# Kernel optimization log

Hardware: AMD Instinct MI355X
Metric: run time of the kernel (lower is better)

## Reference

```python
import jax, jax.numpy as jnp
import numpy as np

B, S, D = 8, 2048, 256
H, DFF, L = 8, 1024, 5
DK = D // H
EPS = 1e-5


def _xavier(key, shape):
    fan_in, fan_out = shape[-2], shape[-1]
    a = jnp.sqrt(6.0 / (fan_in + fan_out))
    return jax.random.uniform(key, shape, jnp.float32, -a, a)


def setup_inputs() -> dict:
    key = jax.random.key(0)
    ks = jax.random.split(key, 12)
    inp = {
        "src": jax.random.normal(ks[0], (B, S, D), jnp.float32),
        "sph": jax.random.normal(ks[1], (B, S, S), jnp.float32),
        # stacked per-layer parameters, leading dim = L
        "Wq": _xavier(ks[2], (L, D, D)), "bq": jnp.zeros((L, D), jnp.float32),
        "Wk": _xavier(ks[3], (L, D, D)), "bk": jnp.zeros((L, D), jnp.float32),
        "Wv": _xavier(ks[4], (L, D, D)), "bv": jnp.zeros((L, D), jnp.float32),
        "Wo": _xavier(ks[5], (L, D, D)), "bo": jnp.zeros((L, D), jnp.float32),
        "W1": _xavier(ks[6], (L, D, DFF)), "b1": jnp.zeros((L, DFF), jnp.float32),
        "W2": _xavier(ks[7], (L, DFF, D)), "b2": jnp.zeros((L, D), jnp.float32),
        "ln1_g": jnp.ones((L, D), jnp.float32), "ln1_b": jnp.zeros((L, D), jnp.float32),
        "ln2_g": jnp.ones((L, D), jnp.float32), "ln2_b": jnp.zeros((L, D), jnp.float32),
    }
    return inp


def _layernorm(x, g, b):
    mu = jnp.mean(x, axis=-1, keepdims=True)
    var = jnp.mean(jnp.square(x - mu), axis=-1, keepdims=True)
    return (x - mu) * jax.lax.rsqrt(var + EPS) * g + b


def _layer(x, sph, Wq, bq, Wk, bk, Wv, bv, Wo, bo, W1, b1, W2, b2, g1, be1, g2, be2):
    # multihead attention with additive sph score bias
    q = (x @ Wq + bq).reshape(B, S, H, DK)
    k = (x @ Wk + bk).reshape(B, S, H, DK)
    v = (x @ Wv + bv).reshape(B, S, H, DK)
    scores = jnp.einsum("bqhd,bkhd->bhqk", q, k) / jnp.sqrt(jnp.float32(DK))
    scores = scores + sph[:, None, :, :]  # bias broadcast over heads
    attn = jax.nn.softmax(scores, axis=-1)
    ctx = jnp.einsum("bhqk,bkhd->bqhd", attn, v).reshape(B, S, D)
    src2 = ctx @ Wo + bo
    x = _layernorm(x + src2, g1, be1)
    # FFN (exact gelu, matching torch F.gelu default)
    h = jax.nn.gelu(x @ W1 + b1, approximate=False)
    src2 = h @ W2 + b2
    x = _layernorm(x + src2, g2, be2)
    return x


def reference(src, sph, Wq, bq, Wk, bk, Wv, bv, Wo, bo, W1, b1, W2, b2, ln1_g, ln1_b, ln2_g, ln2_b):
    x = src
    for i in range(L):
        x = _layer(x, sph, Wq[i], bq[i], Wk[i], bk[i], Wv[i], bv[i], Wo[i], bo[i],
                   W1[i], b1[i], W2[i], b2[i], ln1_g[i], ln1_b[i], ln2_g[i], ln2_b[i])
    return x
```

## Files before the change

### kernel.cpp

```cpp
#include <hip/hip_runtime.h>
#include <cstdint>

__device__ __forceinline__ float b2f(unsigned short u) {
    unsigned int t = ((unsigned int)u) << 16;
    float f;
    __builtin_memcpy(&f, &t, 4);
    return f;
}
__device__ __forceinline__ unsigned short f2b(float f) {
    unsigned int u;
    __builtin_memcpy(&u, &f, 4);
    unsigned int r = (u + 0x7FFFu + ((u >> 16) & 1u)) >> 16;
    return (unsigned short)r;
}
__device__ __forceinline__ float2 bpair(unsigned int u) {
    float2 r;
    unsigned int lo = u << 16;
    unsigned int hi = u & 0xFFFF0000u;
    __builtin_memcpy(&r.x, &lo, 4);
    __builtin_memcpy(&r.y, &hi, 4);
    return r;
}

typedef __attribute__((ext_vector_type(8))) short bf16x8;
typedef __attribute__((ext_vector_type(4))) float f32x4;

#define LOG2E 1.4426950408889634f
#define SC2   0.2550348595f

__device__ __forceinline__ void gload16(const void* g, void* l) {
    __builtin_amdgcn_global_load_lds(
        (const __attribute__((address_space(1))) unsigned int*)g,
        (__attribute__((address_space(3))) unsigned int*)l, 16, 0, 0);
}

__global__ void transcvt_k(const float* __restrict__ in,
                           unsigned short* __restrict__ out, int R, int C,
                           int in_z, int out_z) {
    __shared__ float tile[32][33];
    in += (size_t)blockIdx.z * in_z;
    out += (size_t)blockIdx.z * out_z;
    const int c0 = blockIdx.x * 32, r0 = blockIdx.y * 32;
    const int tx = threadIdx.x, ty = threadIdx.y;
#pragma unroll
    for (int i = 0; i < 32; i += 8)
        tile[ty + i][tx] = in[(size_t)(r0 + ty + i) * C + c0 + tx];
    __syncthreads();
#pragma unroll
    for (int i = 0; i < 32; i += 8)
        out[(size_t)(c0 + ty + i) * R + r0 + tx] = f2b(tile[tx][ty + i]);
}

__global__ __launch_bounds__(256) void sph_cvt(const float* __restrict__ in,
                                               unsigned short* __restrict__ out) {
    const size_t idx = (size_t)blockIdx.x * 256 + threadIdx.x;
    const float4 a = ((const float4*)in)[idx * 2];
    const float4 b = ((const float4*)in)[idx * 2 + 1];
    uint4 o;
    o.x = (unsigned)f2b(a.x * LOG2E) | ((unsigned)f2b(a.y * LOG2E) << 16);
    o.y = (unsigned)f2b(a.z * LOG2E) | ((unsigned)f2b(a.w * LOG2E) << 16);
    o.z = (unsigned)f2b(b.x * LOG2E) | ((unsigned)f2b(b.y * LOG2E) << 16);
    o.w = (unsigned)f2b(b.z * LOG2E) | ((unsigned)f2b(b.w * LOG2E) << 16);
    ((uint4*)out)[idx] = o;
}

__global__ __launch_bounds__(256) void cvt_bf16_k(const float* __restrict__ in,
                                                  unsigned short* __restrict__ out) {
    const size_t idx = (size_t)blockIdx.x * 256 + threadIdx.x;
    const float4 a = ((const float4*)in)[idx * 2];
    const float4 b = ((const float4*)in)[idx * 2 + 1];
    uint4 o;
    o.x = (unsigned)f2b(a.x) | ((unsigned)f2b(a.y) << 16);
    o.y = (unsigned)f2b(a.z) | ((unsigned)f2b(a.w) << 16);
    o.z = (unsigned)f2b(b.x) | ((unsigned)f2b(b.y) << 16);
    o.w = (unsigned)f2b(b.z) | ((unsigned)f2b(b.w) << 16);
    ((uint4*)out)[idx] = o;
}

template <int TN, int QKVB>
__global__ __launch_bounds__(256) void gemm_gl_kernel(
    const unsigned short* __restrict__ A, const unsigned short* __restrict__ Wt,
    const float* __restrict__ biasQ, const float* __restrict__ biasK,
    const float* __restrict__ biasV, unsigned short* __restrict__ C,
    int M, int N, int K, int do_gelu) {
    constexpr int JN = TN / 32;
    constexpr int NCH = 16 + TN / 8;
    __shared__ unsigned short As[128 * 64];
    __shared__ unsigned short Bs[TN * 64];
    const int tid = threadIdx.x;
    const int lane = tid & 63, wid = tid >> 6;
    const int m0 = blockIdx.y * 128, n0 = blockIdx.x * TN;
    const int wm = (wid >> 1) * 64, wn = (wid & 1) * (TN / 2);
    const int quad = lane >> 4, mrow = lane & 15;
    const int lrow = lane >> 3, lslot = lane & 7;
    f32x4 acc[4][JN] = {};

    for (int kb = 0; kb < K; kb += 64) {
#pragma unroll
        for (int cc = 0; cc < NCH / 4; ++cc) {
            const int c = wid * (NCH / 4) + cc;
            if (c < 16) {
                const int row = c * 8 + lrow;
                const int gcol = ((lslot ^ (row & 7)) << 3) + kb;
                gload16(A + (size_t)(m0 + row) * K + gcol, &As[c * 512 + lane * 8]);
            } else {
                const int row = (c - 16) * 8 + lrow;
                const int gcol = ((lslot ^ (row & 7)) << 3) + kb;
                gload16(Wt + (size_t)(n0 + row) * K + gcol, &Bs[(c - 16) * 512 + lane * 8]);
            }
        }
        __syncthreads();
#pragma unroll
        for (int h = 0; h < 2; ++h) {
            bf16x8 af[4], bfr[JN];
#pragma unroll
            for (int i = 0; i < 4; i++) {
                const int ar = wm + i * 16 + mrow;
                af[i] = *(const bf16x8*)&As[ar * 64 + (((h * 4 + quad) ^ (ar & 7)) << 3)];
            }
#pragma unroll
            for (int j = 0; j < JN; j++) {
                const int br = wn + j * 16 + mrow;
                bfr[j] = *(const bf16x8*)&Bs[br * 64 + (((h * 4 + quad) ^ (br & 7)) << 3)];
            }
#pragma unroll
            for (int i = 0; i < 4; i++)
#pragma unroll
                for (int j = 0; j < JN; j++)
                    acc[i][j] = __builtin_amdgcn_mfma_f32_16x16x32_bf16(af[i], bfr[j], acc[i][j], 0, 0, 0);
        }
        __syncthreads();
    }

    const float* bp;
    if (QKVB) {
        const int bsel = n0 >> 8;
        bp = bsel == 0 ? biasQ : (bsel == 1 ? biasK : biasV);
    } else {
        bp = biasQ;
    }
#pragma unroll
    for (int i = 0; i < 4; i++)
#pragma unroll
        for (int j = 0; j < JN; j++) {
            const int col = n0 + wn + j * 16 + mrow;
            const float bv = QKVB ? bp[col & 255] : bp[col];
#pragma unroll
            for (int r = 0; r < 4; r++) {
                const int row = m0 + wm + i * 16 + quad * 4 + r;
                float v = acc[i][j][r] + bv;
                if (do_gelu) v = 0.5f * v * (1.0f + erff(v * 0.70710678118654752f));
                C[(size_t)row * N + col] = f2b(v);
            }
        }
}

template <int SPHB16>
__global__ __launch_bounds__(256) void attn_mfma(
    const unsigned short* __restrict__ Qb, const unsigned short* __restrict__ Kb,
    const unsigned short* __restrict__ Vb, const float* __restrict__ sphf,
    const unsigned short* __restrict__ sphb, unsigned short* __restrict__ Ctx) {
    __shared__ unsigned short Ks[64 * 40];
    __shared__ unsigned short Vt[32 * 72];
    __shared__ unsigned short Ps[4][16 * 72];

    const int tid = threadIdx.x, lane = tid & 63, wid = tid >> 6;
    const int quad = lane >> 4, lq = lane & 15;
    const int bid = blockIdx.x;
    const int h = bid >> 8, b = (bid >> 5) & 7, qt = bid & 31;
    const int q0 = qt * 64;
    const size_t bS = (size_t)b * 2048;

    const int skey = tid >> 2, sdg = (tid & 3) << 3;
    const unsigned short* kgp = Kb + (bS + skey) * 768 + h * 32 + sdg;
    const int vkp = tid & 31, vdg = (tid >> 5) << 2;
    const unsigned short* vgp = Vb + (bS + 2 * vkp) * 768 + h * 32 + vdg;

    const bf16x8 qf = *(const bf16x8*)(Qb + (bS + q0 + wid * 16 + lq) * 768 + h * 32 + quad * 8);

    const size_t sprow = ((size_t)b * 2048 + q0 + wid * 16 + quad * 4) * 2048 + lq;
    const float* spf = sphf + sprow;
    const unsigned short* spb = sphb + sprow;

    float l_r[4] = {0.f, 0.f, 0.f, 0.f};
    f32x4 o0 = {}, o1 = {};

    for (int kt = 0; kt < 32; ++kt) {
        const int k0 = kt * 64;
        __syncthreads();
        *(uint4*)&Ks[skey * 40 + sdg] = *(const uint4*)(kgp + (size_t)k0 * 768);
        {
            uint2 va = *(const uint2*)(vgp + (size_t)k0 * 768);
            uint2 vb2 = *(const uint2*)(vgp + (size_t)k0 * 768 + 768);
            *(unsigned int*)&Vt[(vdg + 0) * 72 + 2 * vkp] = (va.x & 0xFFFFu) | (vb2.x << 16);
            *(unsigned int*)&Vt[(vdg + 1) * 72 + 2 * vkp] = (va.x >> 16) | (vb2.x & 0xFFFF0000u);
            *(unsigned int*)&Vt[(vdg + 2) * 72 + 2 * vkp] = (va.y & 0xFFFFu) | (vb2.y << 16);
            *(unsigned int*)&Vt[(vdg + 3) * 72 + 2 * vkp] = (va.y >> 16) | (vb2.y & 0xFFFF0000u);
        }
        __syncthreads();

        const f32x4 zf = {};
        f32x4 sa0 = __builtin_amdgcn_mfma_f32_16x16x32_bf16(
            qf, *(const bf16x8*)&Ks[(0  + lq) * 40 + quad * 8], zf, 0, 0, 0);
        f32x4 sa1 = __builtin_amdgcn_mfma_f32_16x16x32_bf16(
            qf, *(const bf16x8*)&Ks[(16 + lq) * 40 + quad * 8], zf, 0, 0, 0);
        f32x4 sa2 = __builtin_amdgcn_mfma_f32_16x16x32_bf16(
            qf, *(const bf16x8*)&Ks[(32 + lq) * 40 + quad * 8], zf, 0, 0, 0);
        f32x4 sa3 = __builtin_amdgcn_mfma_f32_16x16x32_bf16(
            qf, *(const bf16x8*)&Ks[(48 + lq) * 40 + quad * 8], zf, 0, 0, 0);

#pragma unroll
        for (int r = 0; r < 4; ++r) {
            float sb0, sb1, sb2, sb3;
            if (SPHB16) {
                const unsigned short* spr = spb + (size_t)r * 2048 + k0;
                sb0 = b2f(spr[0]);  sb1 = b2f(spr[16]);
                sb2 = b2f(spr[32]); sb3 = b2f(spr[48]);
            } else {
                const float* spr = spf + (size_t)r * 2048 + k0;
                sb0 = spr[0]  * LOG2E; sb1 = spr[16] * LOG2E;
                sb2 = spr[32] * LOG2E; sb3 = spr[48] * LOG2E;
            }
            const float p0 = __builtin_amdgcn_exp2f(fmaf(sa0[r], SC2, sb0));
            const float p1 = __builtin_amdgcn_exp2f(fmaf(sa1[r], SC2, sb1));
            const float p2 = __builtin_amdgcn_exp2f(fmaf(sa2[r], SC2, sb2));
            const float p3 = __builtin_amdgcn_exp2f(fmaf(sa3[r], SC2, sb3));
            l_r[r] += (p0 + p1) + (p2 + p3);
            unsigned short* pw = &Ps[wid][(quad * 4 + r) * 72 + lq];
            pw[0]  = f2b(p0);
            pw[16] = f2b(p1);
            pw[32] = f2b(p2);
            pw[48] = f2b(p3);
        }

#pragma unroll
        for (int k2 = 0; k2 < 2; ++k2) {
            bf16x8 pf = *(const bf16x8*)&Ps[wid][lq * 72 + k2 * 32 + quad * 8];
            o0 = __builtin_amdgcn_mfma_f32_16x16x32_bf16(
                pf, *(const bf16x8*)&Vt[(0  + lq) * 72 + k2 * 32 + quad * 8], o0, 0, 0, 0);
            o1 = __builtin_amdgcn_mfma_f32_16x16x32_bf16(
                pf, *(const bf16x8*)&Vt[(16 + lq) * 72 + k2 * 32 + quad * 8], o1, 0, 0, 0);
        }
    }

    unsigned short* op = Ctx + (bS + q0 + wid * 16 + quad * 4) * 256 + h * 32;
#pragma unroll
    for (int r = 0; r < 4; ++r) {
        float l = l_r[r];
        l += __shfl_xor(l, 1);
        l += __shfl_xor(l, 2);
        l += __shfl_xor(l, 4);
        l += __shfl_xor(l, 8);
        const float inv = 1.f / l;
        op[r * 256 + lq]      = f2b(o0[r] * inv);
        op[r * 256 + 16 + lq] = f2b(o1[r] * inv);
    }
}

__global__ __launch_bounds__(256) void add_ln_kernel(
    const float* x, const unsigned short* r,
    const float* __restrict__ g, const float* __restrict__ be,
    float* out, unsigned short* xb) {
    const int lane = threadIdx.x & 63, wid = threadIdx.x >> 6;
    const size_t row = (size_t)blockIdx.x * 4 + wid;
    float4 xv = *(const float4*)(x + row * 256 + lane * 4);
    uint2 ru = *(const uint2*)(r + row * 256 + lane * 4);
    float2 ra = bpair(ru.x), rb = bpair(ru.y);
    float v[4] = {xv.x + ra.x, xv.y + ra.y, xv.z + rb.x, xv.w + rb.y};
    float sum = v[0] + v[1] + v[2] + v[3];
#pragma unroll
    for (int off = 32; off; off >>= 1) sum += __shfl_xor(sum, off);
    const float mu = sum * (1.f / 256.f);
    float sq = 0.f;
#pragma unroll
    for (int i = 0; i < 4; i++) { float d = v[i] - mu; sq += d * d; }
#pragma unroll
    for (int off = 32; off; off >>= 1) sq += __shfl_xor(sq, off);
    const float rs = rsqrtf(sq * (1.f / 256.f) + 1e-5f);
    float4 o;
    o.x = (v[0] - mu) * rs * g[lane * 4 + 0] + be[lane * 4 + 0];
    o.y = (v[1] - mu) * rs * g[lane * 4 + 1] + be[lane * 4 + 1];
    o.z = (v[2] - mu) * rs * g[lane * 4 + 2] + be[lane * 4 + 2];
    o.w = (v[3] - mu) * rs * g[lane * 4 + 3] + be[lane * 4 + 3];
    *(float4*)(out + row * 256 + lane * 4) = o;
    uint2 p;
    p.x = (unsigned)f2b(o.x) | ((unsigned)f2b(o.y) << 16);
    p.y = (unsigned)f2b(o.z) | ((unsigned)f2b(o.w) << 16);
    *(uint2*)(xb + row * 256 + lane * 4) = p;
}

extern "C" void kernel_launch(void* const* d_in, const int* in_sizes, int n_in,
                              void* d_out, int out_size, void* d_ws, size_t ws_size,
                              hipStream_t stream) {
    const float* src = (const float*)d_in[0];
    const float* sph = (const float*)d_in[1];
    const float* Wq  = (const float*)d_in[2];
    const float* bq  = (const float*)d_in[3];
    const float* Wk  = (const float*)d_in[4];
    const float* bk  = (const float*)d_in[5];
    const float* Wv  = (const float*)d_in[6];
    const float* bv  = (const float*)d_in[7];
    const float* Wo  = (const float*)d_in[8];
    const float* bo  = (const float*)d_in[9];
    const float* W1  = (const float*)d_in[10];
    const float* b1  = (const float*)d_in[11];
    const float* W2  = (const float*)d_in[12];
    const float* b2  = (const float*)d_in[13];
    const float* g1  = (const float*)d_in[14];
    const float* be1 = (const float*)d_in[15];
    const float* g2  = (const float*)d_in[16];
    const float* be2 = (const float*)d_in[17];

    char* ws = (char*)d_ws;
    float* X = (float*)d_out;
    unsigned short* QKV = (unsigned short*)(ws + 0);
    unsigned short* CTX = (unsigned short*)(ws + 25165824);
    unsigned short* T2  = (unsigned short*)(ws + 33554432);
    unsigned short* H   = QKV;
    unsigned short* XB  = T2;
    unsigned short* WtQKV = (unsigned short*)(ws + 41943040);
    unsigned short* WtO   = (unsigned short*)(ws + 43909120);
    unsigned short* Wt1   = (unsigned short*)(ws + 44564480);
    unsigned short* Wt2   = (unsigned short*)(ws + 47185920);
    unsigned short* SPHB  = (unsigned short*)(ws + 50331648);
    const int use_b16 = (ws_size >= (size_t)117440512);

    const dim3 tb(32, 8);
    transcvt_k<<<dim3(8, 8, 5),  tb, 0, stream>>>(Wq, WtQKV,          256, 256, 65536, 196608);
    transcvt_k<<<dim3(8, 8, 5),  tb, 0, stream>>>(Wk, WtQKV + 65536,  256, 256, 65536, 196608);
    transcvt_k<<<dim3(8, 8, 5),  tb, 0, stream>>>(Wv, WtQKV + 131072, 256, 256, 65536, 196608);
    transcvt_k<<<dim3(8, 8, 5),  tb, 0, stream>>>(Wo, WtO,            256, 256, 65536, 65536);
    transcvt_k<<<dim3(32, 8, 5), tb, 0, stream>>>(W1, Wt1,            256, 1024, 262144, 262144);
    transcvt_k<<<dim3(8, 32, 5), tb, 0, stream>>>(W2, Wt2,            1024, 256, 262144, 262144);
    if (use_b16) sph_cvt<<<16384, 256, 0, stream>>>(sph, SPHB);
    cvt_bf16_k<<<2048, 256, 0, stream>>>(src, XB);

    hipMemcpyAsync(X, src, 16777216, hipMemcpyDeviceToDevice, stream);

    const int M = 16384;
    for (int lyr = 0; lyr < 5; ++lyr) {
        gemm_gl_kernel<128, 1><<<dim3(6, 128), 256, 0, stream>>>(
            XB, WtQKV + lyr * 196608, bq + lyr * 256, bk + lyr * 256, bv + lyr * 256,
            QKV, M, 768, 256, 0);
        if (use_b16)
            attn_mfma<1><<<2048, 256, 0, stream>>>(QKV, QKV + 256, QKV + 512, sph, SPHB, CTX);
        else
            attn_mfma<0><<<2048, 256, 0, stream>>>(QKV, QKV + 256, QKV + 512, sph, SPHB, CTX);
        gemm_gl_kernel<64, 0><<<dim3(4, 128), 256, 0, stream>>>(
            CTX, WtO + lyr * 65536, bo + lyr * 256, nullptr, nullptr, T2, M, 256, 256, 0);
        add_ln_kernel<<<4096, 256, 0, stream>>>(X, T2, g1 + lyr * 256, be1 + lyr * 256, X, XB);
        gemm_gl_kernel<128, 0><<<dim3(8, 128), 256, 0, stream>>>(
            XB, Wt1 + lyr * 262144, b1 + lyr * 1024, nullptr, nullptr, H, M, 1024, 256, 1);
        gemm_gl_kernel<64, 0><<<dim3(4, 128), 256, 0, stream>>>(
            H, Wt2 + lyr * 262144, b2 + lyr * 256, nullptr, nullptr, T2, M, 256, 1024, 0);
        add_ln_kernel<<<4096, 256, 0, stream>>>(X, T2, g2 + lyr * 256, be2 + lyr * 256, X, XB);
    }
}
```

Measured before the change: 1.493 ms.

## Remap attention blocks, add MFMA priority hints, packed bf16 converts, fuse src copy

Attention blocks are remapped so consecutive block IDs fall on different (b,h) groups. The V-tile load is reordered so each pair of rows sits 16 apart, and K/V pointers are advanced incrementally. s_setprio is raised around the MFMA sections to favour matrix issue. Scalar bf16 rounding is replaced with packed hardware conversion in several kernels, and P is written as 32-bit pairs. The device-to-device memcpy of src is folded into the bf16 conversion kernel. The block remap changes L2 locality for sph and K/V, which could help or hurt.

```diff
diff --git a/kernel.cpp b/kernel.cpp
--- a/kernel.cpp
+++ b/kernel.cpp
@@ -1,4 +1,5 @@
 #include <hip/hip_runtime.h>
+#include <hip/hip_bf16.h>
 #include <cstdint>
 
 __device__ __forceinline__ float b2f(unsigned short u) {
@@ -12,6 +13,12 @@
     __builtin_memcpy(&u, &f, 4);
     unsigned int r = (u + 0x7FFFu + ((u >> 16) & 1u)) >> 16;
     return (unsigned short)r;
+}
+__device__ __forceinline__ unsigned int pkbf(float a, float b) {
+    __hip_bfloat162 t = __float22bfloat162_rn(float2{a, b});
+    unsigned int u;
+    __builtin_memcpy(&u, &t, 4);
+    return u;
 }
 __device__ __forceinline__ float2 bpair(unsigned int u) {
     float2 r;
@@ -57,24 +64,27 @@
     const float4 a = ((const float4*)in)[idx * 2];
     const float4 b = ((const float4*)in)[idx * 2 + 1];
     uint4 o;
-    o.x = (unsigned)f2b(a.x * LOG2E) | ((unsigned)f2b(a.y * LOG2E) << 16);
-    o.y = (unsigned)f2b(a.z * LOG2E) | ((unsigned)f2b(a.w * LOG2E) << 16);
-    o.z = (unsigned)f2b(b.x * LOG2E) | ((unsigned)f2b(b.y * LOG2E) << 16);
-    o.w = (unsigned)f2b(b.z * LOG2E) | ((unsigned)f2b(b.w * LOG2E) << 16);
+    o.x = pkbf(a.x * LOG2E, a.y * LOG2E);
+    o.y = pkbf(a.z * LOG2E, a.w * LOG2E);
+    o.z = pkbf(b.x * LOG2E, b.y * LOG2E);
+    o.w = pkbf(b.z * LOG2E, b.w * LOG2E);
     ((uint4*)out)[idx] = o;
 }
 
 __global__ __launch_bounds__(256) void cvt_bf16_k(const float* __restrict__ in,
-                                                  unsigned short* __restrict__ out) {
+                                                  unsigned short* __restrict__ out,
+                                                  float* __restrict__ xcopy) {
     const size_t idx = (size_t)blockIdx.x * 256 + threadIdx.x;
     const float4 a = ((const float4*)in)[idx * 2];
     const float4 b = ((const float4*)in)[idx * 2 + 1];
     uint4 o;
-    o.x = (unsigned)f2b(a.x) | ((unsigned)f2b(a.y) << 16);
-    o.y = (unsigned)f2b(a.z) | ((unsigned)f2b(a.w) << 16);
-    o.z = (unsigned)f2b(b.x) | ((unsigned)f2b(b.y) << 16);
-    o.w = (unsigned)f2b(b.z) | ((unsigned)f2b(b.w) << 16);
+    o.x = pkbf(a.x, a.y);
+    o.y = pkbf(a.z, a.w);
+    o.z = pkbf(b.x, b.y);
+    o.w = pkbf(b.z, b.w);
     ((uint4*)out)[idx] = o;
+    ((float4*)xcopy)[idx * 2] = a;
+    ((float4*)xcopy)[idx * 2 + 1] = b;
 }
 
 template <int TN, int QKVB>
@@ -166,15 +176,18 @@
 
     const int tid = threadIdx.x, lane = tid & 63, wid = tid >> 6;
     const int quad = lane >> 4, lq = lane & 15;
-    const int bid = blockIdx.x;
+    const int bid0 = blockIdx.x;
+    const int bid = (bid0 & 7) * 256 + (bid0 >> 3);
     const int h = bid >> 8, b = (bid >> 5) & 7, qt = bid & 31;
     const int q0 = qt * 64;
     const size_t bS = (size_t)b * 2048;
 
     const int skey = tid >> 2, sdg = (tid & 3) << 3;
-    const unsigned short* kgp = Kb + (bS + skey) * 768 + h * 32 + sdg;
+    const unsigned short* kp = Kb + (bS + skey) * 768 + h * 32 + sdg;
     const int vkp = tid & 31, vdg = (tid >> 5) << 2;
-    const unsigned short* vgp = Vb + (bS + 2 * vkp) * 768 + h * 32 + vdg;
+    const int vm = vkp & 15, vc = vkp >> 4;
+    const int vso = 2 * vm + 32 * vc;
+    const unsigned short* vp = Vb + (bS + vm + 32 * vc) * 768 + h * 32 + vdg;
 
     const bf16x8 qf = *(const bf16x8*)(Qb + (bS + q0 + wid * 16 + lq) * 768 + h * 32 + quad * 8);
 
@@ -186,20 +199,22 @@
     f32x4 o0 = {}, o1 = {};
 
     for (int kt = 0; kt < 32; ++kt) {
-        const int k0 = kt * 64;
         __syncthreads();
-        *(uint4*)&Ks[skey * 40 + sdg] = *(const uint4*)(kgp + (size_t)k0 * 768);
+        *(uint4*)&Ks[skey * 40 + sdg] = *(const uint4*)kp;
         {
-            uint2 va = *(const uint2*)(vgp + (size_t)k0 * 768);
-            uint2 vb2 = *(const uint2*)(vgp + (size_t)k0 * 768 + 768);
-            *(unsigned int*)&Vt[(vdg + 0) * 72 + 2 * vkp] = (va.x & 0xFFFFu) | (vb2.x << 16);
-            *(unsigned int*)&Vt[(vdg + 1) * 72 + 2 * vkp] = (va.x >> 16) | (vb2.x & 0xFFFF0000u);
-            *(unsigned int*)&Vt[(vdg + 2) * 72 + 2 * vkp] = (va.y & 0xFFFFu) | (vb2.y << 16);
-            *(unsigned int*)&Vt[(vdg + 3) * 72 + 2 * vkp] = (va.y >> 16) | (vb2.y & 0xFFFF0000u);
-        }
+            uint2 va  = *(const uint2*)vp;
+            uint2 vb2 = *(const uint2*)(vp + 16 * 768);
+            *(unsigned int*)&Vt[(vdg + 0) * 72 + vso] = (va.x & 0xFFFFu) | (vb2.x << 16);
+            *(unsigned int*)&Vt[(vdg + 1) * 72 + vso] = (va.x >> 16) | (vb2.x & 0xFFFF0000u);
+            *(unsigned int*)&Vt[(vdg + 2) * 72 + vso] = (va.y & 0xFFFFu) | (vb2.y << 16);
+            *(unsigned int*)&Vt[(vdg + 3) * 72 + vso] = (va.y >> 16) | (vb2.y & 0xFFFF0000u);
+        }
+        kp += 64 * 768;
+        vp += 64 * 768;
         __syncthreads();
 
         const f32x4 zf = {};
+        __builtin_amdgcn_s_setprio(1);
         f32x4 sa0 = __builtin_amdgcn_mfma_f32_16x16x32_bf16(
             qf, *(const bf16x8*)&Ks[(0  + lq) * 40 + quad * 8], zf, 0, 0, 0);
         f32x4 sa1 = __builtin_amdgcn_mfma_f32_16x16x32_bf16(
@@ -208,7 +223,9 @@
             qf, *(const bf16x8*)&Ks[(32 + lq) * 40 + quad * 8], zf, 0, 0, 0);
         f32x4 sa3 = __builtin_amdgcn_mfma_f32_16x16x32_bf16(
             qf, *(const bf16x8*)&Ks[(48 + lq) * 40 + quad * 8], zf, 0, 0, 0);
-
+        __builtin_amdgcn_s_setprio(0);
+
+        const int k0 = kt * 64;
 #pragma unroll
         for (int r = 0; r < 4; ++r) {
             float sb0, sb1, sb2, sb3;
@@ -226,13 +243,12 @@
             const float p2 = __builtin_amdgcn_exp2f(fmaf(sa2[r], SC2, sb2));
             const float p3 = __builtin_amdgcn_exp2f(fmaf(sa3[r], SC2, sb3));
             l_r[r] += (p0 + p1) + (p2 + p3);
-            unsigned short* pw = &Ps[wid][(quad * 4 + r) * 72 + lq];
-            pw[0]  = f2b(p0);
-            pw[16] = f2b(p1);
-            pw[32] = f2b(p2);
-            pw[48] = f2b(p3);
-        }
-
+            unsigned int* pw = (unsigned int*)&Ps[wid][(quad * 4 + r) * 72];
+            pw[lq]      = pkbf(p0, p1);
+            pw[lq + 16] = pkbf(p2, p3);
+        }
+
+        __builtin_amdgcn_s_setprio(1);
 #pragma unroll
         for (int k2 = 0; k2 < 2; ++k2) {
             bf16x8 pf = *(const bf16x8*)&Ps[wid][lq * 72 + k2 * 32 + quad * 8];
@@ -241,6 +257,7 @@
             o1 = __builtin_amdgcn_mfma_f32_16x16x32_bf16(
                 pf, *(const bf16x8*)&Vt[(16 + lq) * 72 + k2 * 32 + quad * 8], o1, 0, 0, 0);
         }
+        __builtin_amdgcn_s_setprio(0);
     }
 
     unsigned short* op = Ctx + (bS + q0 + wid * 16 + quad * 4) * 256 + h * 32;
@@ -284,8 +301,8 @@
     o.w = (v[3] - mu) * rs * g[lane * 4 + 3] + be[lane * 4 + 3];
     *(float4*)(out + row * 256 + lane * 4) = o;
     uint2 p;
-    p.x = (unsigned)f2b(o.x) | ((unsigned)f2b(o.y) << 16);
-    p.y = (unsigned)f2b(o.z) | ((unsigned)f2b(o.w) << 16);
+    p.x = pkbf(o.x, o.y);
+    p.y = pkbf(o.z, o.w);
     *(uint2*)(xb + row * 256 + lane * 4) = p;
 }
 
@@ -333,9 +350,7 @@
     transcvt_k<<<dim3(32, 8, 5), tb, 0, stream>>>(W1, Wt1,            256, 1024, 262144, 262144);
     transcvt_k<<<dim3(8, 32, 5), tb, 0, stream>>>(W2, Wt2,            1024, 256, 262144, 262144);
     if (use_b16) sph_cvt<<<16384, 256, 0, stream>>>(sph, SPHB);
-    cvt_bf16_k<<<2048, 256, 0, stream>>>(src, XB);
-
-    hipMemcpyAsync(X, src, 16777216, hipMemcpyDeviceToDevice, stream);
+    cvt_bf16_k<<<2048, 256, 0, stream>>>(src, XB, X);
 
     const int M = 16384;
     for (int lyr = 0; lyr < 5; ++lyr) {
```

New measurement: 1.436 ms. -3.8%, faster.
